# Optimization experiments

Hardware: AMD Instinct MI355X
Metric: run time of the kernel (lower is better)

The kernel has to match this reference:

```python
import math
import jax, jax.numpy as jnp
import numpy as np

T_MIN = 0.1
T_MAX = 1.0


def _log_cond_prob(energy, text_mask, mel_mask, direction, neg):
    # energy: (B, I, J); returns (B, I, J, K) with K=J (alpha) or J-1 (beta)
    B, I, J = energy.shape
    if direction == 'alpha':
        K = J
        tri_jk = jnp.arange(J)[:, None] >= jnp.arange(K)[None, :]  # torch triu: valid if j >= k
    else:
        K = J - 1
        tri_jk = jnp.arange(J)[:, None] <= jnp.arange(K)[None, :]  # torch tril: valid if j <= k
    tm = text_mask[:, :, None, None]           # (B,I,1,1)
    mmj = mel_mask[:, None, :, None]           # (B,1,J,1)
    mmk = mel_mask[:, None, None, :K]          # (B,1,1,K)
    mask = tm & mmj & mmk                      # (B,I,J,K)
    tri = tri_jk[None, None] & mask
    mask_invalid = jnp.broadcast_to(tm & mmk, (B, I, J, K))
    text_invalid = jnp.broadcast_to(tm, (B, I, J, K))
    right_mask = mask | (~mask_invalid)
    e = jnp.broadcast_to(energy[..., None], (B, I, J, K))
    e = jnp.where((~tri) & mask_invalid, neg, e)
    e = jnp.where(~mask_invalid, -10.0, e)
    e = e - jax.nn.logsumexp(e, axis=2, keepdims=True)  # normalize over mel dim j
    e = jnp.where(~mask_invalid, neg, e)
    e = jnp.where(~right_mask, -10.0, e)
    e = jnp.where(~text_invalid, -10.0, e)
    return e


def _roll(x, shifts, axis):
    # per-batch roll of x along `axis` by shifts[b]
    return jax.vmap(lambda xb, s: jnp.roll(xb, s, axis=axis - 1))(x, shifts)


def _right_shift(x, sh_t, sh_m):
    x = _roll(x, sh_t, 1)
    x = _roll(x, sh_m, 2)
    return _roll(x, sh_m.at[1:].add(-1), 3)  # faithful to in-place shifts_mel_dim[1:] -= 1


def _left_shift(x, sh_t, sh_m):
    x = x[..., None]
    x = _roll(x, -sh_t, 1)
    x = _roll(x, -sh_m, 2)
    return x[..., 0]


def _compute_alpha(lcp_a, neg):
    # alpha[:, i, j] = lse_k(alpha[:, i-1, k] + lcp_a[:, i-1, j-1, k]) for j >= i
    B, I, J, _ = lcp_a.shape
    j_idx = jnp.arange(J + 1)
    row0 = jnp.full((B, J + 1), neg, dtype=lcp_a.dtype).at[:, 0].set(0.0)

    def step(prev, xs):  # prev = alpha[:, i-1, :J]
        lcp_i, i = xs
        new = jax.nn.logsumexp(prev[:, None, :] + lcp_i, axis=2)  # (B, J), index j-1
        row = jnp.concatenate([jnp.full((B, 1), neg, dtype=new.dtype), new], axis=1)
        row = jnp.where(j_idx[None, :] >= i, row, neg)
        return row[:, :J], row

    _, rows = jax.lax.scan(step, row0[:, :J], (jnp.swapaxes(lcp_a, 0, 1), jnp.arange(1, I + 1)))
    return jnp.concatenate([row0[:, None, :], jnp.swapaxes(rows, 0, 1)], axis=1)  # (B, I+1, J+1)


def _compute_beta(lcp_b, neg):
    # beta[:, i, j] = lse_k(beta[:, i+1, k+1] + lcp_b[:, i, j, k]) for j < J+i-I+1
    B, I, J, _ = lcp_b.shape
    j_idx = jnp.arange(J)
    last = jnp.full((B, J), neg, dtype=lcp_b.dtype).at[:, J - 1].set(0.0)

    def step(nxt, xs):
        lcp_i, i = xs
        full = jax.nn.logsumexp(nxt[:, 1:][:, None, :] + lcp_i, axis=2)  # (B, J)
        row = jnp.where(j_idx[None, :] < (J + i - I + 1), full, neg)
        return row, row

    _, rows = jax.lax.scan(step, last, (jnp.swapaxes(lcp_b[:, :I - 1], 0, 1), jnp.arange(I - 1)), reverse=True)
    return jnp.concatenate([jnp.swapaxes(rows, 0, 1), last[:, None, :]], axis=1)  # (B, I, J)


def _forward(text_embeddings, mel_embeddings, text_mask, mel_mask, noise, temperature_ratio, neg):
    B, I, Dt = text_embeddings.shape
    _, J, Dm = mel_embeddings.shape
    energy = jnp.einsum('bid,bjd->bij', text_embeddings, mel_embeddings) / math.sqrt(Dt * Dm)
    temp = T_MIN + (T_MAX - T_MIN) * temperature_ratio[0]
    energy = (energy - jnp.log(-jnp.log(noise))) / temp  # Gumbel noise + temperature
    lcp_a = _log_cond_prob(energy, text_mask, mel_mask, 'alpha', neg)
    alpha = _compute_alpha(lcp_a, neg)
    t_len = text_mask.sum(1)
    m_len = mel_mask.sum(1)
    sh_t = t_len.max() - t_len
    sh_m = m_len.max() - m_len
    lcp_b = _log_cond_prob(energy, text_mask, mel_mask, 'beta', neg)
    lcp_b = _right_shift(lcp_b, sh_t, sh_m)
    beta = _compute_beta(lcp_b, neg)
    beta = _left_shift(beta, sh_t, sh_m)
    gamma = alpha[:, 1:, 1:] + beta
    gamma_mask = text_mask[:, :, None] & mel_mask[:, None, :]
    gls_mask = jnp.broadcast_to(text_mask[:, :, None], (B, I, J)) | gamma_mask
    gamma = jnp.where(gls_mask, gamma, neg)
    gamma = gamma - jax.nn.logsumexp(gamma, axis=1, keepdims=True)  # normalize over text dim
    gamma = jnp.where(gamma_mask, gamma, neg)
    expanded = jnp.einsum('bij,bid->bjd', jnp.exp(gamma), text_embeddings)
    expanded = expanded * mel_mask[:, :, None]
    return gamma, expanded


def setup_inputs() -> dict:
    key = jax.random.key(0)
    k1, k2, k3, k4 = jax.random.split(key, 4)
    B, I, J, Dt, Dm = 1, 128, 640, 256, 256
    text_embeddings = jax.random.normal(k1, (B, I, Dt), dtype=jnp.float32)
    mel_embeddings = jax.random.normal(k2, (B, J, Dm), dtype=jnp.float32)
    text_mask = jnp.ones((B, I), dtype=bool)
    mel_mask = jnp.ones((B, J), dtype=bool)
    noise = jnp.clip(jax.random.uniform(k3, (B, I, J), dtype=jnp.float32), 1e-8, 1.0 - 1e-8)
    temperature_ratio = jax.random.uniform(k4, (1,), dtype=jnp.float32)
    return {
        'text_embeddings': text_embeddings,
        'mel_embeddings': mel_embeddings,
        'text_mask': text_mask,
        'mel_mask': mel_mask,
        'noise': noise,
        'temperature_ratio': temperature_ratio,
    }


def reference(text_embeddings, mel_embeddings, text_mask, mel_mask, noise, temperature_ratio):
    return _forward(text_embeddings, mel_embeddings, text_mask, mel_mask, noise, temperature_ratio, -jnp.inf)
```

## Files before the change

### kernel.cpp

```cpp
#include <hip/hip_runtime.h>
#include <math.h>

constexpr int TI = 128;
constexpr int TJ = 640;
constexpr int TD = 256;
constexpr int EPL = 10;

#define NEG (-1e30f)
#define LOG2E 1.44269504088896340736f
#define LN2   0.69314718055994530942f

__device__ __forceinline__ float rexp2(float x) { return __builtin_amdgcn_exp2f(x); }
__device__ __forceinline__ float rlog2(float x) { return __builtin_amdgcn_logf(x); }

struct MS { float m, s; };
__device__ __forceinline__ MS ms_combine(MS a, MS b) {
    float d = b.m - a.m;
    bool al = d <= 0.0f;
    float m = al ? a.m : b.m;
    float t = rexp2(al ? d : -d);
    float s = al ? fmaf(b.s, t, a.s) : fmaf(a.s, t, b.s);
    return {m, s};
}
__device__ __forceinline__ MS ms_push(MS run, float x) { return ms_combine(run, {x, 1.0f}); }
__device__ __forceinline__ float ms_final(MS a) {
    return (a.m < -1e29f) ? NEG : a.m + rlog2(a.s);
}

template<int CTRL, int RMASK>
__device__ __forceinline__ float dpp_f(float src, float oldv) {
    int r = __builtin_amdgcn_update_dpp(
        __float_as_int(oldv), __float_as_int(src), CTRL, RMASK, 0xF, false);
    return __int_as_float(r);
}
template<int CTRL, int RMASK>
__device__ __forceinline__ MS dpp_ms(MS v) {
    MS t;
    t.m = dpp_f<CTRL, RMASK>(v.m, NEG);
    t.s = dpp_f<CTRL, RMASK>(v.s, 0.0f);
    return t;
}
__device__ __forceinline__ MS wave_incl_scan_ms(MS v) {
    v = ms_combine(dpp_ms<0x111, 0xF>(v), v);
    v = ms_combine(dpp_ms<0x112, 0xF>(v), v);
    v = ms_combine(dpp_ms<0x114, 0xF>(v), v);
    v = ms_combine(dpp_ms<0x118, 0xF>(v), v);
    v = ms_combine(dpp_ms<0x142, 0xA>(v), v);
    v = ms_combine(dpp_ms<0x143, 0xC>(v), v);
    return v;
}
__device__ __forceinline__ MS wave_excl_from_incl_ms(MS incl) {
    return dpp_ms<0x138, 0xF>(incl);
}
__device__ __forceinline__ float wave_incl_scan_add(float v) {
    v += dpp_f<0x111, 0xF>(v, 0.0f);
    v += dpp_f<0x112, 0xF>(v, 0.0f);
    v += dpp_f<0x114, 0xF>(v, 0.0f);
    v += dpp_f<0x118, 0xF>(v, 0.0f);
    v += dpp_f<0x142, 0xA>(v, 0.0f);
    v += dpp_f<0x143, 0xC>(v, 0.0f);
    return v;
}
__device__ __forceinline__ float wave_incl_scan_max(float v) {
    v = fmaxf(v, dpp_f<0x111, 0xF>(v, NEG));
    v = fmaxf(v, dpp_f<0x112, 0xF>(v, NEG));
    v = fmaxf(v, dpp_f<0x114, 0xF>(v, NEG));
    v = fmaxf(v, dpp_f<0x118, 0xF>(v, NEG));
    v = fmaxf(v, dpp_f<0x142, 0xA>(v, NEG));
    v = fmaxf(v, dpp_f<0x143, 0xC>(v, NEG));
    return v;
}
__device__ __forceinline__ float readlane63(float v) {
    return __int_as_float(__builtin_amdgcn_readlane(__float_as_int(v), 63));
}
__device__ __forceinline__ float readlaneN(float v, int n) {
    return __int_as_float(__builtin_amdgcn_readlane(__float_as_int(v), n));
}

__global__ __launch_bounds__(256) void k_melT(
        const float* __restrict__ mel, float* __restrict__ melT) {
    __shared__ float ldsT[64][65];
    int j0 = blockIdx.x * 64, c0 = blockIdx.y * 64, tid = threadIdx.x;
    int rr = tid >> 4, c4 = tid & 15;
    #pragma unroll
    for (int p = 0; p < 4; p++) {
        int r = p * 16 + rr;
        float4 v = *(const float4*)(mel + (size_t)(j0 + r) * TD + c0 + c4 * 4);
        ldsT[c4 * 4 + 0][r] = v.x;
        ldsT[c4 * 4 + 1][r] = v.y;
        ldsT[c4 * 4 + 2][r] = v.z;
        ldsT[c4 * 4 + 3][r] = v.w;
    }
    __syncthreads();
    int jj = tid & 63, cw = tid >> 6;
    #pragma unroll
    for (int p = 0; p < 16; p++) {
        int cc = p * 4 + cw;
        melT[(size_t)(c0 + cc) * TJ + j0 + jj] = ldsT[cc][jj];
    }
}

__global__ __launch_bounds__(640) void k_energy(
        const float* __restrict__ text, const float* __restrict__ melT,
        const float* __restrict__ noise, const float* __restrict__ trat,
        float* __restrict__ energy, float* __restrict__ Ga,
        float* __restrict__ Gb, float* __restrict__ Cst) {
    __shared__ float trowm[TD], trowc[TD], trowp[TD];
    __shared__ float erowm[TJ], erowc[TJ], erowp[TJ];
    __shared__ float pcur[TJ], scur[TJ];
    __shared__ float wred[2][EPL];
    int i = blockIdx.x, tid = threadIdx.x;
    if (tid < TD) {
        trowc[tid] = text[i * TD + tid];
        trowm[tid] = (i > 0)      ? text[(i - 1) * TD + tid] : 0.0f;
        trowp[tid] = (i < TI - 1) ? text[(i + 1) * TD + tid] : 0.0f;
    }
    __syncthreads();
    float temp = 0.1f + 0.9f * trat[0];
    float sc = LOG2E / temp;
    int j = tid;
    float am = 0.0f, ac = 0.0f, ap = 0.0f;
    #pragma unroll 8
    for (int c = 0; c < TD; c++) {
        float m = melT[(size_t)c * TJ + j];
        am = fmaf(trowm[c], m, am);
        ac = fmaf(trowc[c], m, ac);
        ap = fmaf(trowp[c], m, ap);
    }
    float gm = (i > 0)      ? logf(-logf(noise[(i - 1) * TJ + j])) : 0.0f;
    float gc =                logf(-logf(noise[i * TJ + j]));
    float gp = (i < TI - 1) ? logf(-logf(noise[(i + 1) * TJ + j])) : 0.0f;
    erowm[j] = (am * (1.0f / 256.0f) - gm) * sc;
    float e2 = (ac * (1.0f / 256.0f) - gc) * sc;
    erowc[j] = e2;
    erowp[j] = (ap * (1.0f / 256.0f) - gp) * sc;
    energy[i * TJ + j] = e2;
    __syncthreads();
    if (tid < 64) {
        int l = tid;
        MS loc = {NEG, 0.0f};
        #pragma unroll
        for (int q = 0; q < EPL; q++) loc = ms_push(loc, erowc[l * EPL + q]);
        MS off = wave_excl_from_incl_ms(wave_incl_scan_ms(loc));
        MS run = off;
        #pragma unroll
        for (int q = 0; q < EPL; q++) {
            run = ms_push(run, erowc[l * EPL + q]);
            pcur[l * EPL + q] = ms_final(run);
        }
        loc = {NEG, 0.0f};
        #pragma unroll
        for (int q = 0; q < EPL; q++) loc = ms_push(loc, erowc[TJ - 1 - (l * EPL + q)]);
        off = wave_excl_from_incl_ms(wave_incl_scan_ms(loc));
        run = off;
        #pragma unroll
        for (int q = 0; q < EPL; q++) {
            int idx = TJ - 1 - (l * EPL + q);
            run = ms_push(run, erowc[idx]);
            scur[idx] = ms_final(run);
        }
    }
    __syncthreads();
    float ga, gb;
    if (i == 0) ga = (j == 0) ? -scur[0] : NEG;
    else        ga = (j == 0) ? NEG : erowm[j - 1] - scur[j];
    bool has_b = (i <= TI - 2);
    if (has_b) {
        if (i == TI - 2) gb = (j == 1) ? -pcur[TJ - 2] : NEG;
        else             gb = (j == 0) ? NEG : erowp[TJ - j] - pcur[TJ - 1 - j];
    } else gb = NEG;
    int wv = tid >> 6, l = tid & 63;
    float ma = readlane63(wave_incl_scan_max(ga));
    float mb = readlane63(wave_incl_scan_max(gb));
    if (l == 0) { wred[0][wv] = ma; wred[1][wv] = mb; }
    __syncthreads();
    float Ca = wred[0][0], Cb = wred[1][0];
    #pragma unroll
    for (int k = 1; k < EPL; k++) {
        Ca = fmaxf(Ca, wred[0][k]);
        Cb = fmaxf(Cb, wred[1][k]);
    }
    Ga[i * TJ + j] = rexp2(ga - Ca);
    if (has_b) Gb[i * TJ + j] = rexp2(gb - Cb);
    if (tid == 0) { Cst[i] = Ca; if (has_b) Cst[TI + i] = Cb; }
}

__global__ __launch_bounds__(64, 1) void k_scan(
        const float* __restrict__ Ga, const float* __restrict__ Gb,
        const float* __restrict__ Cst,
        float* __restrict__ PpA, float* __restrict__ PpB,
        float* __restrict__ baseA, float* __restrict__ baseB) {
    constexpr int PF = 6;
    const int l = threadIdx.x;
    const bool is_alpha = (blockIdx.x == 0);
    const int nrows = is_alpha ? TI : TI - 1;
    const float* Gsrc = is_alpha ? Ga : Gb;
    float* Pdst = is_alpha ? PpA : PpB;
    float* bdst = is_alpha ? baseA : baseB;
    const int goff = l * EPL;

    float C0, C1;
    if (is_alpha) { C0 = Cst[l];       C1 = Cst[64 + l]; }
    else          { C0 = Cst[128 + l]; C1 = Cst[192 + l]; }

    float2 gr[PF][5];
    #pragma unroll
    for (int s = 0; s < PF; s++) {
        int row = is_alpha ? s : (TI - 2 - s);
        const float2* gp = (const float2*)(Gsrc + (size_t)row * TJ + goff);
        #pragma unroll
        for (int k = 0; k < 5; k++) gr[s][k] = gp[k];
    }

    float Pp[EPL];
    #pragma unroll
    for (int q = 0; q < EPL; q++) Pp[q] = 0.0f;
    float rprev = 0.0f, Lam = 0.0f;

    for (int tb = 0; tb < nrows; tb += PF) {
        #pragma unroll
        for (int s = 0; s < PF; s++) {
            int t = tb + s;
            if (t < nrows) {
                float gv[EPL];
                #pragma unroll
                for (int k = 0; k < 5; k++) {
                    gv[2*k] = gr[s][k].x; gv[2*k+1] = gr[s][k].y;
                }
                float lp[EPL];
                if (t == 0) {
                    #pragma unroll
                    for (int q = 0; q < EPL; q++) lp[q] = gv[q];
                } else {
                    float carry = dpp_f<0x138, 0xF>(Pp[EPL - 1], 0.0f);
                    float rp = rprev;
                    lp[0] = carry * rp * gv[0];
                    #pragma unroll
                    for (int q = 1; q < EPL; q++) lp[q] = Pp[q - 1] * rp * gv[q];
                }
                #pragma unroll
                for (int q = 9; q >= 1; q--) lp[q] += lp[q - 1];
                #pragma unroll
                for (int q = 9; q >= 2; q--) lp[q] += lp[q - 2];
                #pragma unroll
                for (int q = 9; q >= 4; q--) lp[q] += lp[q - 4];
                #pragma unroll
                for (int q = 9; q >= 8; q--) lp[q] += lp[q - 8];
                float incl = wave_incl_scan_add(lp[EPL - 1]);
                float excl = dpp_f<0x138, 0xF>(incl, 0.0f);
                #pragma unroll
                for (int q = 0; q < EPL; q++) Pp[q] = excl + lp[q];
                float T = readlane63(incl);
                int idx2 = is_alpha ? t : (126 - t);
                float Cc = (idx2 < 64) ? readlaneN(C0, idx2) : readlaneN(C1, idx2 - 64);
                float basev = Lam + Cc;

                float2* dp = (float2*)(Pdst + (size_t)t * TJ + goff);
                #pragma unroll
                for (int k = 0; k < 5; k++) {
                    float2 tv; tv.x = Pp[2*k]; tv.y = Pp[2*k+1];
                    dp[k] = tv;
                }
                if (l == 0) bdst[t] = basev;

                Lam = basev + rlog2(T);
                rprev = (T > 0.0f) ? __builtin_amdgcn_rcpf(T) : 0.0f;

                int tp = t + PF;
                if (tp < nrows) {
                    int rowp = is_alpha ? tp : (TI - 2 - tp);
                    const float2* gp = (const float2*)(Gsrc + (size_t)rowp * TJ + goff);
                    #pragma unroll
                    for (int k = 0; k < 5; k++) gr[s][k] = gp[k];
                }
            }
        }
    }
}

__global__ __launch_bounds__(256) void k_gamma(
        const float* __restrict__ PpA, const float* __restrict__ PpB,
        const float* __restrict__ baseA, const float* __restrict__ baseB,
        const float* __restrict__ energy, const float* __restrict__ text,
        float* __restrict__ outg, float* __restrict__ oute) {
    __shared__ float w128[TI];
    __shared__ float redm[2], reds[2];
    int j = blockIdx.x, tid = threadIdx.x;
    float gg = NEG;
    if (tid < TI) {
        float ev = energy[tid * TJ + j];
        float av = ev + rlog2(PpA[tid * TJ + j]) + baseA[tid];
        float bv;
        if (tid == TI - 1) {
            bv = (j == TJ - 1) ? 0.0f : NEG;
        } else {
            int t = TI - 2 - tid;
            bv = ev + rlog2(PpB[(size_t)t * TJ + (TJ - 1 - j)]) + baseB[t];
        }
        gg = (av < -1e29f || bv < -1e29f) ? NEG : av + bv;
        MS v = {gg, 1.0f};
        #pragma unroll
        for (int off = 32; off > 0; off >>= 1) {
            float om = __shfl_xor(v.m, off, 64);
            float os = __shfl_xor(v.s, off, 64);
            v = ms_combine(v, {om, os});
        }
        if ((tid & 63) == 0) { redm[tid >> 6] = v.m; reds[tid >> 6] = v.s; }
    }
    __syncthreads();
    float lse = ms_final(ms_combine({redm[0], reds[0]}, {redm[1], reds[1]}));
    if (tid < TI) {
        bool fin = gg > -1e29f;
        outg[tid * TJ + j] = fin ? (gg - lse) * LN2 : NEG;
        w128[tid] = fin ? rexp2(gg - lse) : 0.0f;
    }
    __syncthreads();
    float acc = 0.0f;
    #pragma unroll 8
    for (int ii = 0; ii < TI; ii++) acc += w128[ii] * text[ii * TD + tid];
    oute[(size_t)j * TD + tid] = acc;
}

extern "C" void kernel_launch(void* const* d_in, const int* in_sizes, int n_in,
                              void* d_out, int out_size, void* d_ws, size_t ws_size,
                              hipStream_t stream) {
    const float* text  = (const float*)d_in[0];
    const float* mel   = (const float*)d_in[1];
    const float* noise = (const float*)d_in[4];
    const float* trat  = (const float*)d_in[5];

    float* outg = (float*)d_out;
    float* oute = outg + TI * TJ;

    float* w      = (float*)d_ws;
    float* energy = w;
    float* Ga     = w + 1 * TI * TJ;
    float* Gb     = w + 2 * TI * TJ;
    float* Cst    = Gb + (size_t)(TI - 1) * TJ;
    float* baseA  = Cst + 320;
    float* baseB  = Cst + 448;
    float* melT   = w + 3 * TI * TJ;
    float* PpA    = w + 3 * TI * TJ;
    float* PpB    = w + 4 * TI * TJ;

    k_melT  <<<dim3(TJ / 64, TD / 64), 256, 0, stream>>>(mel, melT);
    k_energy<<<TI, TJ, 0, stream>>>(text, melT, noise, trat, energy, Ga, Gb, Cst);
    k_scan  <<<2, 64, 0, stream>>>(Ga, Gb, Cst, PpA, PpB, baseA, baseB);
    k_gamma <<<TJ, 256, 0, stream>>>(PpA, PpB, baseA, baseB, energy, text, outg, oute);
}
```

Baseline: 134.4 us.

## Hand-schedule scan kernel loads with inline asm and explicit vmcnt waits

Rewrites the serial k_scan row loop so that loads and stores are issued through inline asm. Each row waits only on its own prefetched loads via a counted s_waitcnt vmcnt, rather than letting the compiler insert conservative waits. The prefetch depth goes from 6 to 7 rows, stores are widened to dwordx4, and the per-row base value is kept in registers and written once at the end. The goal is to hide global memory latency on this latency-bound single-wave scan. In exchange it hardcodes vmcnt counts that must exactly match the issued load/store sequence, which makes the kernel fragile to any later edit.

```diff
diff --git a/kernel.cpp b/kernel.cpp
--- a/kernel.cpp
+++ b/kernel.cpp
@@ -9,6 +9,9 @@
 #define NEG (-1e30f)
 #define LOG2E 1.44269504088896340736f
 #define LN2   0.69314718055994530942f
+
+typedef float f32x2 __attribute__((ext_vector_type(2)));
+typedef float f32x4 __attribute__((ext_vector_type(4)));
 
 __device__ __forceinline__ float rexp2(float x) { return __builtin_amdgcn_exp2f(x); }
 __device__ __forceinline__ float rlog2(float x) { return __builtin_amdgcn_logf(x); }
@@ -190,7 +193,7 @@
         const float* __restrict__ Cst,
         float* __restrict__ PpA, float* __restrict__ PpB,
         float* __restrict__ baseA, float* __restrict__ baseB) {
-    constexpr int PF = 6;
+    constexpr int PF = 7;
     const int l = threadIdx.x;
     const bool is_alpha = (blockIdx.x == 0);
     const int nrows = is_alpha ? TI : TI - 1;
@@ -199,83 +202,131 @@
     float* bdst = is_alpha ? baseA : baseB;
     const int goff = l * EPL;
 
+#define LOADROW(S, PTR)                                                        \
+    asm volatile("global_load_dwordx2 %0, %5, off\n\t"                         \
+                 "global_load_dwordx2 %1, %5, off offset:8\n\t"                \
+                 "global_load_dwordx2 %2, %5, off offset:16\n\t"               \
+                 "global_load_dwordx2 %3, %5, off offset:24\n\t"               \
+                 "global_load_dwordx2 %4, %5, off offset:32"                   \
+                 : "=&v"(gr[S][0]), "=&v"(gr[S][1]), "=&v"(gr[S][2]),          \
+                   "=&v"(gr[S][3]), "=&v"(gr[S][4])                            \
+                 : "v"(PTR))
+
     float C0, C1;
-    if (is_alpha) { C0 = Cst[l];       C1 = Cst[64 + l]; }
-    else          { C0 = Cst[128 + l]; C1 = Cst[192 + l]; }
-
-    float2 gr[PF][5];
-    #pragma unroll
-    for (int s = 0; s < PF; s++) {
-        int row = is_alpha ? s : (TI - 2 - s);
-        const float2* gp = (const float2*)(Gsrc + (size_t)row * TJ + goff);
-        #pragma unroll
-        for (int k = 0; k < 5; k++) gr[s][k] = gp[k];
+    {
+        const float* c0p = Cst + (is_alpha ? 0 : 128) + l;
+        const float* c1p = c0p + 64;
+        asm volatile("global_load_dword %0, %2, off\n\t"
+                     "global_load_dword %1, %3, off"
+                     : "=&v"(C0), "=&v"(C1) : "v"(c0p), "v"(c1p));
+        asm volatile("s_waitcnt vmcnt(0)" ::: "memory");
+        __builtin_amdgcn_sched_barrier(0);
+    }
+
+    f32x2 gr[PF][5];
+    {
+        const float* gp0 = Gsrc + (size_t)(is_alpha ? 0 : TI - 2) * TJ + goff;
+        const float* gp1 = Gsrc + (size_t)(is_alpha ? 1 : TI - 3) * TJ + goff;
+        const float* gp2 = Gsrc + (size_t)(is_alpha ? 2 : TI - 4) * TJ + goff;
+        const float* gp3 = Gsrc + (size_t)(is_alpha ? 3 : TI - 5) * TJ + goff;
+        const float* gp4 = Gsrc + (size_t)(is_alpha ? 4 : TI - 6) * TJ + goff;
+        const float* gp5 = Gsrc + (size_t)(is_alpha ? 5 : TI - 7) * TJ + goff;
+        const float* gp6 = Gsrc + (size_t)(is_alpha ? 6 : TI - 8) * TJ + goff;
+        LOADROW(0, gp0); LOADROW(1, gp1); LOADROW(2, gp2); LOADROW(3, gp3);
+        LOADROW(4, gp4); LOADROW(5, gp5); LOADROW(6, gp6);
     }
 
     float Pp[EPL];
     #pragma unroll
     for (int q = 0; q < EPL; q++) Pp[q] = 0.0f;
     float rprev = 0.0f, Lam = 0.0f;
-
-    for (int tb = 0; tb < nrows; tb += PF) {
-        #pragma unroll
-        for (int s = 0; s < PF; s++) {
-            int t = tb + s;
-            if (t < nrows) {
-                float gv[EPL];
-                #pragma unroll
-                for (int k = 0; k < 5; k++) {
-                    gv[2*k] = gr[s][k].x; gv[2*k+1] = gr[s][k].y;
-                }
-                float lp[EPL];
-                if (t == 0) {
-                    #pragma unroll
-                    for (int q = 0; q < EPL; q++) lp[q] = gv[q];
-                } else {
-                    float carry = dpp_f<0x138, 0xF>(Pp[EPL - 1], 0.0f);
-                    float rp = rprev;
-                    lp[0] = carry * rp * gv[0];
-                    #pragma unroll
-                    for (int q = 1; q < EPL; q++) lp[q] = Pp[q - 1] * rp * gv[q];
-                }
-                #pragma unroll
-                for (int q = 9; q >= 1; q--) lp[q] += lp[q - 1];
-                #pragma unroll
-                for (int q = 9; q >= 2; q--) lp[q] += lp[q - 2];
-                #pragma unroll
-                for (int q = 9; q >= 4; q--) lp[q] += lp[q - 4];
-                #pragma unroll
-                for (int q = 9; q >= 8; q--) lp[q] += lp[q - 8];
-                float incl = wave_incl_scan_add(lp[EPL - 1]);
-                float excl = dpp_f<0x138, 0xF>(incl, 0.0f);
-                #pragma unroll
-                for (int q = 0; q < EPL; q++) Pp[q] = excl + lp[q];
-                float T = readlane63(incl);
-                int idx2 = is_alpha ? t : (126 - t);
-                float Cc = (idx2 < 64) ? readlaneN(C0, idx2) : readlaneN(C1, idx2 - 64);
-                float basev = Lam + Cc;
-
-                float2* dp = (float2*)(Pdst + (size_t)t * TJ + goff);
-                #pragma unroll
-                for (int k = 0; k < 5; k++) {
-                    float2 tv; tv.x = Pp[2*k]; tv.y = Pp[2*k+1];
-                    dp[k] = tv;
-                }
-                if (l == 0) bdst[t] = basev;
-
-                Lam = basev + rlog2(T);
-                rprev = (T > 0.0f) ? __builtin_amdgcn_rcpf(T) : 0.0f;
-
-                int tp = t + PF;
-                if (tp < nrows) {
-                    int rowp = is_alpha ? tp : (TI - 2 - tp);
-                    const float2* gp = (const float2*)(Gsrc + (size_t)rowp * TJ + goff);
-                    #pragma unroll
-                    for (int k = 0; k < 5; k++) gr[s][k] = gp[k];
-                }
-            }
-        }
-    }
+    float bacc0 = 0.0f, bacc1 = 0.0f;
+
+#define ROWBODY(S, T, KLIT, IS_FIRST)                                          \
+    {                                                                          \
+        asm volatile("s_waitcnt vmcnt(" KLIT ")" ::: "memory");                \
+        __builtin_amdgcn_sched_barrier(0);                                     \
+        float gv[EPL];                                                         \
+        _Pragma("unroll")                                                      \
+        for (int k = 0; k < 5; k++) {                                          \
+            gv[2 * k] = gr[S][k][0]; gv[2 * k + 1] = gr[S][k][1];              \
+        }                                                                      \
+        {   \
+            int tp = (T) + PF;                                                 \
+            int rpi = (tp < nrows) ? tp : (nrows - 1);                         \
+            int rowp = is_alpha ? rpi : (TI - 2 - rpi);                        \
+            const float* gpn = Gsrc + (size_t)rowp * TJ + goff;                \
+            LOADROW(S, gpn);                                                   \
+        }                                                                      \
+        float lp[EPL];                                                         \
+        if (IS_FIRST) {                                                        \
+            _Pragma("unroll")                                                  \
+            for (int q = 0; q < EPL; q++) lp[q] = gv[q];                       \
+        } else {                                                               \
+            float carry = dpp_f<0x138, 0xF>(Pp[EPL - 1], 0.0f);                \
+            float rp = rprev;                                                  \
+            lp[0] = carry * rp * gv[0];                                        \
+            _Pragma("unroll")                                                  \
+            for (int q = 1; q < EPL; q++) lp[q] = Pp[q - 1] * rp * gv[q];      \
+        }                                                                      \
+        _Pragma("unroll")                                                      \
+        for (int q = 9; q >= 1; q--) lp[q] += lp[q - 1];                       \
+        _Pragma("unroll")                                                      \
+        for (int q = 9; q >= 2; q--) lp[q] += lp[q - 2];                       \
+        _Pragma("unroll")                                                      \
+        for (int q = 9; q >= 4; q--) lp[q] += lp[q - 4];                       \
+        _Pragma("unroll")                                                      \
+        for (int q = 9; q >= 8; q--) lp[q] += lp[q - 8];                       \
+        float incl = wave_incl_scan_add(lp[EPL - 1]);                          \
+        float excl = dpp_f<0x138, 0xF>(incl, 0.0f);                            \
+        _Pragma("unroll")                                                      \
+        for (int q = 0; q < EPL; q++) Pp[q] = excl + lp[q];                    \
+        float T_ = readlane63(incl);                                           \
+        int idx2 = is_alpha ? (T) : (126 - (T));                               \
+        float Cc = (idx2 < 64) ? readlaneN(C0, idx2)                           \
+                               : readlaneN(C1, idx2 - 64);                     \
+        float basev = Lam + Cc;                                                \
+        {            \
+            f32x4 p03, p47; f32x2 p89;                                         \
+            p03[0] = Pp[0]; p03[1] = Pp[1]; p03[2] = Pp[2]; p03[3] = Pp[3];    \
+            p47[0] = Pp[4]; p47[1] = Pp[5]; p47[2] = Pp[6]; p47[3] = Pp[7];    \
+            p89[0] = Pp[8]; p89[1] = Pp[9];                                    \
+            float* pp = Pdst + (size_t)(T) * TJ + goff;                        \
+            asm volatile("global_store_dwordx4 %0, %1, off\n\t"                \
+                         "global_store_dwordx4 %0, %2, off offset:16\n\t"      \
+                         "global_store_dwordx2 %0, %3, off offset:32"          \
+                         :: "v"(pp), "v"(p03), "v"(p47), "v"(p89) : "memory"); \
+        }                                                                      \
+        bacc0 = ((T) == l)      ? basev : bacc0;                               \
+        bacc1 = ((T) == 64 + l) ? basev : bacc1;                               \
+        Lam = basev + rlog2(T_);                                               \
+        rprev = (T_ > 0.0f) ? __builtin_amdgcn_rcpf(T_) : 0.0f;                \
+    }
+
+    ROWBODY(0, 0, "30", true);
+    ROWBODY(1, 1, "33", false);
+    ROWBODY(2, 2, "36", false);
+    ROWBODY(3, 3, "39", false);
+    ROWBODY(4, 4, "42", false);
+    ROWBODY(5, 5, "45", false);
+    ROWBODY(6, 6, "48", false);
+
+    for (int tb = PF; tb < nrows; tb += PF) {
+        { int t = tb + 0; if (t < nrows) ROWBODY(0, t, "51", false); }
+        { int t = tb + 1; if (t < nrows) ROWBODY(1, t, "51", false); }
+        { int t = tb + 2; if (t < nrows) ROWBODY(2, t, "51", false); }
+        { int t = tb + 3; if (t < nrows) ROWBODY(3, t, "51", false); }
+        { int t = tb + 4; if (t < nrows) ROWBODY(4, t, "51", false); }
+        { int t = tb + 5; if (t < nrows) ROWBODY(5, t, "51", false); }
+        { int t = tb + 6; if (t < nrows) ROWBODY(6, t, "51", false); }
+    }
+
+    asm volatile("s_waitcnt vmcnt(0)" ::: "memory");
+    __builtin_amdgcn_sched_barrier(0);
+    bdst[l] = bacc0;
+    bdst[64 + l] = bacc1;
+#undef ROWBODY
+#undef LOADROW
 }
 
 __global__ __launch_bounds__(256) void k_gamma(
```

New measurement: 124.9 us. 1.08x faster.
